# Performance work log

Hardware: AMD Instinct MI355X
Metric: run time of the kernel (lower is better)

Reference implementation:

```python
import jax, jax.numpy as jnp
import numpy as np

DISCOUNT = 0.99
HORIZON = 16


def setup_inputs() -> dict:
    key = jax.random.key(0)
    k1, k2, k3 = jax.random.split(key, 3)
    T, B = 1024, 4096
    rewards = jax.random.normal(k1, (T, B), dtype=jnp.float32)
    values = jax.random.normal(k2, (T, B), dtype=jnp.float32)
    masks = jax.random.uniform(k3, (T, B), dtype=jnp.float32)
    return {"rewards": rewards, "values": values, "masks": masks}


def _n_step_return(rewards, values, masks, gamma, horizon):
    # rewards/values/masks: [T, B]; time_axis == 0
    T = rewards.shape[0]
    rm = rewards * masks  # masked rewards
    # Pad end of time axis with zeros so every window has length `horizon`;
    # out-of-range rewards contribute 0, matching the truncated MC sum.
    pad = jnp.zeros((horizon - 1,) + rm.shape[1:], rm.dtype)
    rm_p = jnp.concatenate([rm, pad], axis=0)  # [T + horizon - 1, B]
    t = jnp.arange(T)
    idx = t[:, None] + jnp.arange(horizon)[None, :]  # [T, horizon]
    windows = rm_p[idx]  # [T, horizon, B]
    disc = jnp.asarray(gamma, rm.dtype) ** jnp.arange(horizon, dtype=rm.dtype)
    g = jnp.einsum('thb,h->tb', windows, disc)  # windowed discounted sums
    # Bootstrap: gamma^{effective_horizon} * V(s_{min(t+horizon-1, T-1)})
    eff_h = (jnp.minimum(t + horizon, T) - t).astype(rm.dtype)  # [T]
    v_idx = jnp.minimum(t + horizon - 1, T - 1)  # [T]
    g = g + (jnp.asarray(gamma, rm.dtype) ** eff_h)[:, None] * values[v_idx]
    return g


def reference(rewards, values, masks):
    return _n_step_return(rewards, values, masks, DISCOUNT, HORIZON)
```

## Files before the change

kernel.cpp:

```cpp
#include <hip/hip_runtime.h>


constexpr int   T_DIM  = 1024;
constexpr int   B_DIM  = 4096;
constexpr int   H      = 16;
constexpr int   CT     = 32;
constexpr float GAMMA  = 0.99f;

constexpr float gpow_c(int n) {
    float g = 1.0f;
    for (int i = 0; i < n; ++i) g *= GAMMA;
    return g;
}
constexpr float G16 = gpow_c(16);

__global__ __launch_bounds__(256)
void NStepReturn_88691074662796_kernel(const float* __restrict__ rewards,
                                       const float* __restrict__ values,
                                       const float* __restrict__ masks,
                                       float* __restrict__ out)
{
    const int b  = blockIdx.x * 256 + threadIdx.x;
    const int t0 = blockIdx.y * CT;
    const int t_last = t0 + CT - 1;

    float buf[H];
    float W = 0.0f;

    #pragma unroll
    for (int h = H - 1; h >= 0; --h) {
        const int t = t_last + h;
        float x = 0.0f;
        if (t < T_DIM) {
            x = rewards[t * B_DIM + b] * masks[t * B_DIM + b];
        }
        buf[(CT - 1 + h) & (H - 1)] = x;
        W = x + GAMMA * W;
    }

    {
        const int t = t_last;
        float gb = G16;
        if (t + H > T_DIM) {
            gb = 1.0f;
            for (int k = 0; k < T_DIM - t; ++k) gb *= GAMMA;
        }
        const int vi = min(t + H - 1, T_DIM - 1);
        out[t * B_DIM + b] = W + gb * values[vi * B_DIM + b];
    }

    #pragma unroll
    for (int j = CT - 2; j >= 0; --j) {
        const int t = t0 + j;
        const float x16 = buf[j & (H - 1)];
        const float x   = rewards[t * B_DIM + b] * masks[t * B_DIM + b];
        buf[j & (H - 1)] = x;
        W = x + GAMMA * W - G16 * x16;

        float gb = G16;
        if (t + H > T_DIM) {
            gb = 1.0f;
            for (int k = 0; k < T_DIM - t; ++k) gb *= GAMMA;
        }
        const int vi = min(t + H - 1, T_DIM - 1);
        out[t * B_DIM + b] = W + gb * values[vi * B_DIM + b];
    }
}

extern "C" void kernel_launch(void* const* d_in, const int* in_sizes, int n_in,
                              void* d_out, int out_size, void* d_ws, size_t ws_size,
                              hipStream_t stream) {
    const float* rewards = (const float*)d_in[0];
    const float* values  = (const float*)d_in[1];
    const float* masks   = (const float*)d_in[2];
    float* out = (float*)d_out;

    dim3 grid(B_DIM / 256, T_DIM / CT);
    dim3 block(256);
    NStepReturn_88691074662796_kernel<<<grid, block, 0, stream>>>(rewards, values, masks, out);
}
```

Baseline: 98.73 us.

## Stage masked rewards in LDS tiles and split time rows across threads

Each block now loads a 79x64 tile of rewards*masks into shared memory once. Eight thread groups each compute eight consecutive outputs from that tile with a sliding-window recurrence, and bootstrap values are prefetched into registers. This cuts the halo re-read overhead from 15/32 to 15/64 per tile and raises parallelism along the time axis. The cost is a shared-memory round trip, a block barrier, and a warm-up sum of 16 terms for every 8 outputs.

```diff
diff --git a/kernel.cpp b/kernel.cpp
--- a/kernel.cpp
+++ b/kernel.cpp
@@ -1,11 +1,14 @@
 #include <hip/hip_runtime.h>
 
 
-constexpr int   T_DIM  = 1024;
-constexpr int   B_DIM  = 4096;
-constexpr int   H      = 16;
-constexpr int   CT     = 32;
-constexpr float GAMMA  = 0.99f;
+constexpr int   T_DIM    = 1024;
+constexpr int   B_DIM    = 4096;
+constexpr int   H        = 16;
+constexpr int   COLS     = 64;
+constexpr int   ROWS_OUT = 64;
+constexpr int   ROWS_LDS = ROWS_OUT + H - 1;
+constexpr int   BLOCK    = 512;
+constexpr float GAMMA    = 0.99f;
 
 constexpr float gpow_c(int n) {
     float g = 1.0f;
@@ -14,56 +17,74 @@
 }
 constexpr float G16 = gpow_c(16);
 
-__global__ __launch_bounds__(256)
+__global__ __launch_bounds__(BLOCK, 8)
 void NStepReturn_88691074662796_kernel(const float* __restrict__ rewards,
                                        const float* __restrict__ values,
                                        const float* __restrict__ masks,
                                        float* __restrict__ out)
 {
-    const int b  = blockIdx.x * 256 + threadIdx.x;
-    const int t0 = blockIdx.y * CT;
-    const int t_last = t0 + CT - 1;
+    __shared__ float rm[ROWS_LDS * COLS];
 
-    float buf[H];
-    float W = 0.0f;
+    const int c0  = blockIdx.x * COLS;
+    const int t0  = blockIdx.y * ROWS_OUT;
+    const int tid = threadIdx.x;
+
+    const int c     = tid & (COLS - 1);
+    const int s     = tid >> 6;
+    const int tbase = t0 + s * 8;
+
+    float v[8];
+    #pragma unroll
+    for (int j = 0; j < 8; ++j) {
+        const int vi = min(tbase + j + H - 1, T_DIM - 1);
+        v[j] = values[vi * B_DIM + c0 + c];
+    }
 
     #pragma unroll
+    for (int base = 0; base < ROWS_LDS * COLS; base += BLOCK) {
+        const int j = base + tid;
+        if (j < ROWS_LDS * COLS) {
+            const int i  = j >> 6;
+            const int cc = j & (COLS - 1);
+            const int t  = t0 + i;
+            float x = 0.0f;
+            if (t < T_DIM) {
+                x = rewards[t * B_DIM + c0 + cc] * masks[t * B_DIM + c0 + cc];
+            }
+            rm[j] = x;
+        }
+    }
+    __syncthreads();
+
+    const float* col = &rm[(s * 8) * COLS + c];
+
+    float W = 0.0f;
+    #pragma unroll
     for (int h = H - 1; h >= 0; --h) {
-        const int t = t_last + h;
-        float x = 0.0f;
-        if (t < T_DIM) {
-            x = rewards[t * B_DIM + b] * masks[t * B_DIM + b];
-        }
-        buf[(CT - 1 + h) & (H - 1)] = x;
-        W = x + GAMMA * W;
+        W = col[(7 + h) * COLS] + GAMMA * W;
     }
 
     {
-        const int t = t_last;
+        const int t = tbase + 7;
         float gb = G16;
         if (t + H > T_DIM) {
             gb = 1.0f;
             for (int k = 0; k < T_DIM - t; ++k) gb *= GAMMA;
         }
-        const int vi = min(t + H - 1, T_DIM - 1);
-        out[t * B_DIM + b] = W + gb * values[vi * B_DIM + b];
+        out[t * B_DIM + c0 + c] = W + gb * v[7];
     }
 
     #pragma unroll
-    for (int j = CT - 2; j >= 0; --j) {
-        const int t = t0 + j;
-        const float x16 = buf[j & (H - 1)];
-        const float x   = rewards[t * B_DIM + b] * masks[t * B_DIM + b];
-        buf[j & (H - 1)] = x;
-        W = x + GAMMA * W - G16 * x16;
+    for (int j = 6; j >= 0; --j) {
+        W = col[j * COLS] + GAMMA * W - G16 * col[(j + H) * COLS];
 
+        const int t = tbase + j;
         float gb = G16;
         if (t + H > T_DIM) {
             gb = 1.0f;
             for (int k = 0; k < T_DIM - t; ++k) gb *= GAMMA;
         }
-        const int vi = min(t + H - 1, T_DIM - 1);
-        out[t * B_DIM + b] = W + gb * values[vi * B_DIM + b];
+        out[t * B_DIM + c0 + c] = W + gb * v[j];
     }
 }
 
@@ -75,7 +96,7 @@
     const float* masks   = (const float*)d_in[2];
     float* out = (float*)d_out;
 
-    dim3 grid(B_DIM / 256, T_DIM / CT);
-    dim3 block(256);
+    dim3 grid(B_DIM / COLS, T_DIM / ROWS_OUT);
+    dim3 block(BLOCK);
     NStepReturn_88691074662796_kernel<<<grid, block, 0, stream>>>(rewards, values, masks, out);
 }
```

Result: faster. 92.93 us (-5.9%).
